# Kernel tuning notes

Measured on AMD Instinct MI355X. Metric: run time of the kernel, lower is better.

## Reference

```python
import jax, jax.numpy as jnp
import numpy as np
import math

B, T, D, NH, HD = 2, 1024, 768, 12, 64
V, L, E, CAP_F, H = 50257, 2, 8, 1.25, 2048
AUX_W, Z_W, THETA, EPS = 0.01, 0.001, 10000.0, 1e-5
N = B * T
CAP = int(math.ceil(N / E * CAP_F))  # 320


def setup_inputs():
    key = jax.random.key(0)
    ks = jax.random.split(key, 8)
    s = 0.02
    return dict(
        idx=jax.random.randint(ks[0], (B, T), 0, V),
        wte=jax.random.normal(ks[1], (V, D), jnp.float32) * s,
        wqkv=jax.random.normal(ks[2], (L, D, 3 * D), jnp.float32) * s,
        q_norm_w=jnp.ones((L, D), jnp.float32),
        k_norm_w=jnp.ones((L, D), jnp.float32),
        o_proj=jax.random.normal(ks[3], (L, D, D), jnp.float32) * s,
        ffn_norm_w=jnp.ones((L, D), jnp.float32),
        gate_w=jax.random.normal(ks[4], (L, D, E), jnp.float32) * s,
        w13=jax.random.normal(ks[5], (L, E, D, 2 * H), jnp.float32) * s,
        w2=jax.random.normal(ks[6], (L, E, H, D), jnp.float32) * s,
        ln_f_w=jnp.ones((D,), jnp.float32),
    )


def rmsnorm(x, w):
    return x * jax.lax.rsqrt(jnp.mean(x * x, axis=-1, keepdims=True) + EPS) * w


def rope(x, cos, sin):
    # x: (B, nh, T, HD) viewed as complex pairs on last dim
    xr = x.reshape(*x.shape[:-1], HD // 2, 2)
    x0, x1 = xr[..., 0], xr[..., 1]
    out = jnp.stack([x0 * cos - x1 * sin, x0 * sin + x1 * cos], axis=-1)
    return out.reshape(x.shape)


def moe(x, gate_w, w13, w2):
    # x: (B, T, D) -> Switch MoE (k=1) with capacity CAP and token drops
    x_flat = x.reshape(N, D).astype(jnp.float32)
    logits = x_flat @ gate_w  # (N, E) fp32
    probs = jax.nn.softmax(logits, axis=-1)
    top = jnp.argmax(logits, axis=-1)  # (N,)
    prob_mass = probs.mean(axis=0)
    fraction = jax.nn.one_hot(top, E, dtype=jnp.float32).mean(axis=0)
    balance_loss = jnp.sum(prob_mass * fraction) * AUX_W * E
    z = jax.nn.logsumexp(logits, axis=-1)
    z_loss = jnp.mean(z * z) * Z_W
    aux = balance_loss + z_loss

    sort_idx = jnp.argsort(top)  # stable
    sorted_assign = top[sort_idx]
    counts = jnp.bincount(sorted_assign, length=E)
    offsets = jnp.concatenate([jnp.zeros((1,), counts.dtype), jnp.cumsum(counts)])[:E]
    rank = jnp.arange(N) - offsets[sorted_assign]  # position within expert segment
    keep = rank < CAP
    x_perm = x_flat[sort_idx]
    slot = jnp.where(keep, rank, CAP)  # dropped -> overflow slot
    buf = jnp.zeros((E, CAP + 1, D), jnp.float32).at[sorted_assign, slot].set(x_perm)
    xb = buf[:, :CAP]  # (E, CAP, D)
    gu = jnp.einsum('ecd,edh->ech', xb, w13)  # (E, CAP, 2H)
    g, u = jnp.split(gu, 2, axis=-1)
    y = jnp.einsum('ech,ehd->ecd', jax.nn.silu(g) * u, w2)  # (E, CAP, D)
    out_perm = y[sorted_assign, jnp.minimum(rank, CAP - 1)] * keep[:, None]
    out_flat = jnp.zeros((N, D), jnp.float32).at[sort_idx].set(out_perm)
    return out_flat.reshape(B, T, D), aux, top.reshape(B, T), keep[jnp.argsort(sort_idx)].reshape(B, T)


def forward(idx, wte, wqkv, q_norm_w, k_norm_w, o_proj, ffn_norm_w, gate_w, w13, w2, ln_f_w):
    x = wte[idx]  # (B, T, D)
    freqs = 1.0 / (THETA ** (jnp.arange(0, HD, 2, dtype=jnp.float32) / HD))
    ang = jnp.outer(jnp.arange(T, dtype=jnp.float32), freqs)  # (T, HD//2)
    cos, sin = jnp.cos(ang)[None, None], jnp.sin(ang)[None, None]
    mask = jnp.where(jnp.tril(jnp.ones((T, T), bool)), 0.0, -jnp.inf)
    aux_total = jnp.float32(0.0)
    for l in range(L):
        qkv = x @ wqkv[l]
        q, k, v = jnp.split(qkv, 3, axis=-1)
        q = rmsnorm(q, q_norm_w[l])
        k = rmsnorm(k, k_norm_w[l])
        q = q.reshape(B, T, NH, HD).transpose(0, 2, 1, 3)
        k = k.reshape(B, T, NH, HD).transpose(0, 2, 1, 3)
        v = v.reshape(B, T, NH, HD).transpose(0, 2, 1, 3)
        q, k = rope(q, cos, sin), rope(k, cos, sin)
        scores = jnp.einsum('bhqd,bhkd->bhqk', q, k) / math.sqrt(HD) + mask
        attn = jax.nn.softmax(scores, axis=-1)
        y = jnp.einsum('bhqk,bhkd->bhqd', attn, v).transpose(0, 2, 1, 3).reshape(B, T, D)
        h = x + y @ o_proj[l]
        ffn_in = rmsnorm(h, ffn_norm_w[l])
        moe_out, aux, _, _ = moe(ffn_in, gate_w[l], w13[l], w2[l])
        aux_total = aux_total + aux
        x = h + moe_out
    x = rmsnorm(x, ln_f_w)
    logits = x @ wte.T  # tied lm_head
    return logits, aux_total


def reference(idx, wte, wqkv, q_norm_w, k_norm_w, o_proj, ffn_norm_w, gate_w, w13, w2, ln_f_w):
    return forward(idx, wte, wqkv, q_norm_w, k_norm_w, o_proj, ffn_norm_w, gate_w, w13, w2, ln_f_w)
```

## Files before the change

kernel.cpp:

```cpp
#include <hip/hip_runtime.h>

typedef __attribute__((ext_vector_type(8))) _Float16 half8;
typedef __attribute__((ext_vector_type(4))) float f32x4;

constexpr int Bc = 2, Tc = 1024, Dc = 768, NHc = 12, HDc = 64;
constexpr int Vc = 50257, Lc = 2, Ec = 8, Hc = 2048;
constexpr int Ntok = Bc * Tc;
constexpr int CAPc = 320, CAPPc = 384;
constexpr long long LOGITS_N = (long long)Bc * Tc * Vc;

typedef const __attribute__((address_space(1))) unsigned int* gas_t;
typedef __attribute__((address_space(3))) unsigned int* las_t;
__device__ __forceinline__ void gload16(const void* g, void* l) {
  __builtin_amdgcn_global_load_lds((gas_t)g, (las_t)l, 16, 0, 0);
}

__device__ __forceinline__ void splitf16(float a, unsigned short& h, unsigned short& l) {
  _Float16 hh = (_Float16)a;
  _Float16 ll = (_Float16)(a - (float)hh);
  h = __builtin_bit_cast(unsigned short, hh);
  l = __builtin_bit_cast(unsigned short, ll);
}
__device__ __forceinline__ unsigned short f16o(float a) {
  _Float16 hh = (_Float16)a;
  return __builtin_bit_cast(unsigned short, hh);
}


__global__ void zero_small(float* psum, float* z2) {
  int t = threadIdx.x;
  if (t < Lc * Ec) psum[t] = 0.f;
  if (t < Lc) z2[t] = 0.f;
}

__global__ void embed_k(const int* __restrict__ idx, const float* __restrict__ wte,
                        float* __restrict__ x, unsigned short* __restrict__ x16) {
  int n = blockIdx.x;
  long long v = idx[n];
  const float4* src = (const float4*)(wte + v * 768);
  float4* dst = (float4*)(x + (long long)n * 768);
  int t = threadIdx.x;
  if (t < 192) {
    float4 val = src[t];
    dst[t] = val;
    ushort4 h, l;
    splitf16(val.x, h.x, l.x); splitf16(val.y, h.y, l.y);
    splitf16(val.z, h.z, l.z); splitf16(val.w, h.w, l.w);
    unsigned short* d = x16 + (long long)n * 1536 + t * 4;
    *(ushort4*)d = h;
    *(ushort4*)(d + 768) = l;
  }
}

__global__ void f2h4(const float* __restrict__ in, unsigned short* __restrict__ out,
                     long long n4) {
  long long i = (long long)blockIdx.x * 256 + threadIdx.x;
  if (i >= n4) return;
  float4 v = ((const float4*)in)[i];
  ushort4 o;
  o.x = f16o(v.x); o.y = f16o(v.y); o.z = f16o(v.z); o.w = f16o(v.w);
  ((ushort4*)out)[i] = o;
}

template <int SP>
__global__ void __launch_bounds__(256) split2_wT(const float* __restrict__ src,
    unsigned short* __restrict__ dst, int K, int N, long long sS, long long sD) {
  __shared__ float t[32][33];
  int z = blockIdx.z;
  src += (long long)z * sS;
  dst += (long long)z * sD;
  int n0 = blockIdx.x * 32, k0 = blockIdx.y * 32;
  int tid = threadIdx.x;
  int r = tid >> 3, c4 = (tid & 7) * 4;
  float4 v = *(const float4*)(src + (long long)(k0 + r) * N + n0 + c4);
  t[r][c4 + 0] = v.x; t[r][c4 + 1] = v.y; t[r][c4 + 2] = v.z; t[r][c4 + 3] = v.w;
  __syncthreads();
  int n = tid >> 3, kq = (tid & 7) * 4;
  ushort4 h, l;
  splitf16(t[kq + 0][n], h.x, l.x);
  splitf16(t[kq + 1][n], h.y, l.y);
  splitf16(t[kq + 2][n], h.z, l.z);
  splitf16(t[kq + 3][n], h.w, l.w);
  const int lda = SP ? 2 * K : K;
  unsigned short* d = dst + (long long)(n0 + n) * lda + k0 + kq;
  *(ushort4*)d = h;
  if (SP) *(ushort4*)(d + K) = l;
}

__global__ void __launch_bounds__(256) rmsnorm_k(const float* in, int istride,
                                                 float* outp, int ostride,
                                                 const float* w) {
  long long n = blockIdx.x;
  const float* xr = in + n * istride;
  float* yr = outp + n * ostride;
  int tid = threadIdx.x;
  float s = 0.f;
  for (int i = tid; i < 768; i += 256) { float v = xr[i]; s += v * v; }
  #pragma unroll
  for (int o = 32; o; o >>= 1) s += __shfl_down(s, o);
  __shared__ float red[4];
  __shared__ float bs;
  if ((tid & 63) == 0) red[tid >> 6] = s;
  __syncthreads();
  if (tid == 0) bs = rsqrtf((red[0] + red[1] + red[2] + red[3]) / 768.0f + 1e-5f);
  __syncthreads();
  float sc = bs;
  for (int i = tid; i < 768; i += 256) yr[i] = xr[i] * sc * w[i];
}

__global__ void __launch_bounds__(256) rmsnorm_h(const float* in,
                                                 unsigned short* outp, const float* w) {
  long long n = blockIdx.x;
  const float* xr = in + n * 768;
  unsigned short* yr = outp + n * 768;
  int tid = threadIdx.x;
  float s = 0.f;
  for (int i = tid; i < 768; i += 256) { float v = xr[i]; s += v * v; }
  #pragma unroll
  for (int o = 32; o; o >>= 1) s += __shfl_down(s, o);
  __shared__ float red[4];
  __shared__ float bs;
  if ((tid & 63) == 0) red[tid >> 6] = s;
  __syncthreads();
  if (tid == 0) bs = rsqrtf((red[0] + red[1] + red[2] + red[3]) / 768.0f + 1e-5f);
  __syncthreads();
  float sc = bs;
  for (int i = tid; i < 768; i += 256) yr[i] = f16o(xr[i] * sc * w[i]);
}

__global__ void __launch_bounds__(256) qk_rope(const float* __restrict__ qkv,
    const float* __restrict__ qnw, const float* __restrict__ knw,
    unsigned short* __restrict__ qr, unsigned short* __restrict__ kr,
    unsigned short* __restrict__ vr) {
  int n = blockIdx.x;
  int t = n & 1023, b = n >> 10;
  const float* row = qkv + (long long)n * 2304;
  int tid = threadIdx.x;
  float sq = 0.f, sk = 0.f;
  for (int i = tid; i < 768; i += 256) {
    float q = row[i]; sq += q * q;
    float k = row[768 + i]; sk += k * k;
  }
  #pragma unroll
  for (int o = 32; o; o >>= 1) { sq += __shfl_down(sq, o); sk += __shfl_down(sk, o); }
  __shared__ float redq[4], redk[4];
  __shared__ float bq, bk;
  if ((tid & 63) == 0) { redq[tid >> 6] = sq; redk[tid >> 6] = sk; }
  __syncthreads();
  if (tid == 0) {
    bq = rsqrtf((redq[0] + redq[1] + redq[2] + redq[3]) / 768.0f + 1e-5f);
    bk = rsqrtf((redk[0] + redk[1] + redk[2] + redk[3]) / 768.0f + 1e-5f);
  }
  __syncthreads();
  float nq = bq, nk = bk;
  for (int i = tid; i < 384; i += 256) {
    int hh = i >> 5, j = i & 31;
    int c = hh * 64 + 2 * j;
    float ang = (float)t * powf(10000.0f, -((float)j * (1.0f / 32.0f)));
    float cs = cosf(ang), sn = sinf(ang);
    int z = b * 12 + hh;
    long long qb = ((long long)z * 1024 + t) * 128 + 2 * j;
    unsigned short h0, l0, h1, l1;
    float q0 = row[c] * nq * qnw[c], q1 = row[c + 1] * nq * qnw[c + 1];
    splitf16(q0 * cs - q1 * sn, h0, l0);
    splitf16(q0 * sn + q1 * cs, h1, l1);
    *(unsigned int*)&qr[qb] = (unsigned)h0 | ((unsigned)h1 << 16);
    *(unsigned int*)&qr[qb + 64] = (unsigned)l0 | ((unsigned)l1 << 16);
    float k0 = row[768 + c] * nk * knw[c], k1 = row[768 + c + 1] * nk * knw[c + 1];
    splitf16(k0 * cs - k1 * sn, h0, l0);
    splitf16(k0 * sn + k1 * cs, h1, l1);
    *(unsigned int*)&kr[qb] = (unsigned)h0 | ((unsigned)h1 << 16);
    *(unsigned int*)&kr[qb + 64] = (unsigned)l0 | ((unsigned)l1 << 16);
    splitf16(row[1536 + c], h0, l0);
    splitf16(row[1536 + c + 1], h1, l1);
    long long vb = ((long long)z * 64 + 2 * j) * 2048 + t;
    vr[vb] = h0; vr[vb + 1024] = l0;
    vr[vb + 2048] = h1; vr[vb + 3072] = l1;
  }
}

__global__ void __launch_bounds__(256) flash_attn(
    const unsigned short* __restrict__ qr, const unsigned short* __restrict__ kr,
    const unsigned short* __restrict__ vr, unsigned short* __restrict__ yout) {
  __shared__ __align__(16) unsigned short Ph[4][16][72];
  __shared__ __align__(16) unsigned short Pl[4][16][72];
  int bid = blockIdx.x;
  int z = bid >> 4;
  int qt = 15 - (bid & 15);
  int b = z / 12, h = z % 12;
  int q0 = qt * 64;
  int wave = threadIdx.x >> 6, lane = threadIdx.x & 63;
  int lr = lane & 15, lg = lane >> 4;
  int qw = q0 + wave * 16;
  half8 af[2][2];
  const unsigned short* qbase = qr + ((long long)z * 1024 + qw + lr) * 128;
  #pragma unroll
  for (int ks = 0; ks < 2; ++ks)
    #pragma unroll
    for (int p = 0; p < 2; ++p)
      af[ks][p] = *(const half8*)(qbase + p * 64 + ks * 32 + lg * 8);
  f32x4 accy[4];
  #pragma unroll
  for (int df = 0; df < 4; ++df) accy[df] = (f32x4){0.f, 0.f, 0.f, 0.f};
  float mrun[4] = {-3.4e38f, -3.4e38f, -3.4e38f, -3.4e38f};
  float srun[4] = {0.f, 0.f, 0.f, 0.f};
  for (int kt = 0; kt <= qt; ++kt) {
    int kv0 = kt * 64;
    f32x4 s[4];
    #pragma unroll
    for (int nf = 0; nf < 4; ++nf) s[nf] = (f32x4){0.f, 0.f, 0.f, 0.f};
    const unsigned short* kbase = kr + ((long long)z * 1024 + kv0 + lr) * 128;
    #pragma unroll
    for (int nf = 0; nf < 4; ++nf) {
      const unsigned short* kb = kbase + nf * 16 * 128;
      #pragma unroll
      for (int ks = 0; ks < 2; ++ks) {
        half8 bh = *(const half8*)(kb + ks * 32 + lg * 8);
        half8 bl = *(const half8*)(kb + 64 + ks * 32 + lg * 8);
        s[nf] = __builtin_amdgcn_mfma_f32_16x16x32_f16(af[ks][0], bh, s[nf], 0, 0, 0);
        s[nf] = __builtin_amdgcn_mfma_f32_16x16x32_f16(af[ks][1], bh, s[nf], 0, 0, 0);
        s[nf] = __builtin_amdgcn_mfma_f32_16x16x32_f16(af[ks][0], bl, s[nf], 0, 0, 0);
      }
    }
    bool diag = (kt == qt);
    #pragma unroll
    for (int nf = 0; nf < 4; ++nf)
      #pragma unroll
      for (int j = 0; j < 4; ++j) {
        float v = s[nf][j] * 0.125f;
        if (diag && (nf * 16 + lr > wave * 16 + lg * 4 + j)) v = -1e30f;
        s[nf][j] = v;
      }
    #pragma unroll
    for (int j = 0; j < 4; ++j) {
      float tm = fmaxf(fmaxf(s[0][j], s[1][j]), fmaxf(s[2][j], s[3][j]));
      #pragma unroll
      for (int o = 1; o < 16; o <<= 1) tm = fmaxf(tm, __shfl_xor(tm, o));
      float mnew = fmaxf(mrun[j], tm);
      float sc = expf(mrun[j] - mnew);
      float ts = 0.f;
      #pragma unroll
      for (int nf = 0; nf < 4; ++nf) {
        float p = expf(s[nf][j] - mnew);
        ts += p;
        unsigned short ph, pl;
        splitf16(p, ph, pl);
        Ph[wave][lg * 4 + j][nf * 16 + lr] = ph;
        Pl[wave][lg * 4 + j][nf * 16 + lr] = pl;
      }
      #pragma unroll
      for (int o = 1; o < 16; o <<= 1) ts += __shfl_xor(ts, o);
      srun[j] = srun[j] * sc + ts;
      mrun[j] = mnew;
      #pragma unroll
      for (int df = 0; df < 4; ++df) accy[df][j] *= sc;
    }
    #pragma unroll
    for (int ks2 = 0; ks2 < 2; ++ks2) {
      half8 aph = *(const half8*)&Ph[wave][lr][ks2 * 32 + lg * 8];
      half8 apl = *(const half8*)&Pl[wave][lr][ks2 * 32 + lg * 8];
      #pragma unroll
      for (int df = 0; df < 4; ++df) {
        const unsigned short* vb =
            vr + ((long long)z * 64 + df * 16 + lr) * 2048 + kv0 + ks2 * 32 + lg * 8;
        half8 bvh = *(const half8*)vb;
        half8 bvl = *(const half8*)(vb + 1024);
        accy[df] = __builtin_amdgcn_mfma_f32_16x16x32_f16(aph, bvh, accy[df], 0, 0, 0);
        accy[df] = __builtin_amdgcn_mfma_f32_16x16x32_f16(apl, bvh, accy[df], 0, 0, 0);
        accy[df] = __builtin_amdgcn_mfma_f32_16x16x32_f16(aph, bvl, accy[df], 0, 0, 0);
      }
    }
  }
  float inv[4];
  #pragma unroll
  for (int j = 0; j < 4; ++j) inv[j] = 1.0f / srun[j];
  #pragma unroll
  for (int df = 0; df < 4; ++df)
    #pragma unroll
    for (int j = 0; j < 4; ++j) {
      long long tok = (long long)b * 1024 + qw + lg * 4 + j;
      int col = h * 64 + df * 16 + lr;
      unsigned short hh, ll;
      splitf16(accy[df][j] * inv[j], hh, ll);
      yout[tok * 1536 + col] = hh;
      yout[tok * 1536 + 768 + col] = ll;
    }
}

__global__ void __launch_bounds__(256) gate_k(const float* __restrict__ xin,
    const float* __restrict__ gw, int* __restrict__ top,
    float* __restrict__ psum, float* __restrict__ z2) {
  __shared__ float gws[768 * 8];
  __shared__ float pacc[8];
  __shared__ float zacc;
  int tid = threadIdx.x;
  for (int i = tid; i < 768 * 8 / 4; i += 256) ((float4*)gws)[i] = ((const float4*)gw)[i];
  if (tid < 8) pacc[tid] = 0.f;
  if (tid == 0) zacc = 0.f;
  __syncthreads();
  int n = blockIdx.x * 256 + tid;
  const float4* xr4 = (const float4*)(xin + (long long)n * 768);
  float l[8] = {0, 0, 0, 0, 0, 0, 0, 0};
  for (int d4 = 0; d4 < 192; ++d4) {
    float4 xv = xr4[d4];
    const float* g = &gws[d4 * 32];
    #pragma unroll
    for (int e = 0; e < 8; ++e)
      l[e] += xv.x * g[e] + xv.y * g[8 + e] + xv.z * g[16 + e] + xv.w * g[24 + e];
  }
  float mx = l[0]; int bi = 0;
  #pragma unroll
  for (int e = 1; e < 8; ++e) if (l[e] > mx) { mx = l[e]; bi = e; }
  float p[8]; float se = 0.f;
  #pragma unroll
  for (int e = 0; e < 8; ++e) { p[e] = expf(l[e] - mx); se += p[e]; }
  float z = mx + logf(se);
  top[n] = bi;
  #pragma unroll
  for (int e = 0; e < 8; ++e) atomicAdd(&pacc[e], p[e] / se);
  atomicAdd(&zacc, z * z);
  __syncthreads();
  if (tid < 8) atomicAdd(&psum[tid], pacc[tid]);
  if (tid == 0) atomicAdd(z2, zacc);
}

__global__ void route_scan(const int* __restrict__ top, int* __restrict__ rank,
                           int* __restrict__ cnt) {
  int lane = threadIdx.x;
  int c[8] = {0, 0, 0, 0, 0, 0, 0, 0};
  unsigned long long below = (1ull << lane) - 1ull;
  for (int s = 0; s < Ntok / 64; ++s) {
    int n = s * 64 + lane;
    int e = top[n];
    int r = 0;
    #pragma unroll
    for (int q = 0; q < 8; ++q) {
      unsigned long long m = __ballot(e == q);
      if (e == q) r = c[q] + __popcll(m & below);
      c[q] += __popcll(m);
    }
    rank[n] = r;
  }
  #pragma unroll
  for (int q = 0; q < 8; ++q) if (lane == q) cnt[q] = c[q];
}

template <int SP>
__global__ void scatter_xb(const float* __restrict__ xin, const int* __restrict__ top,
                           const int* __restrict__ rank, unsigned short* __restrict__ xb) {
  int n = blockIdx.x;
  int r = rank[n];
  if (r >= CAPc) return;
  int e = top[n];
  int t = threadIdx.x;
  if (t >= 192) return;
  float4 v = ((const float4*)(xin + (long long)n * 768))[t];
  ushort4 h, l;
  splitf16(v.x, h.x, l.x); splitf16(v.y, h.y, l.y);
  splitf16(v.z, h.z, l.z); splitf16(v.w, h.w, l.w);
  const int lda = SP ? 1536 : 768;
  unsigned short* dst = xb + ((long long)e * CAPPc + r) * lda + t * 4;
  *(ushort4*)dst = h;
  if (SP) *(ushort4*)(dst + 768) = l;
}

template <int SP>
__global__ void __launch_bounds__(256) silu_k(const float* __restrict__ gu,
                                              unsigned short* __restrict__ act) {
  long long i = (long long)blockIdx.x * 256 + threadIdx.x;
  long long row = i >> 11;
  int h = (int)(i & 2047);
  float g = gu[row * 4096 + h];
  float u = gu[row * 4096 + 2048 + h];
  float a = g / (1.f + expf(-g)) * u;
  if (SP) {
    unsigned short hh, ll;
    splitf16(a, hh, ll);
    act[row * 4096 + h] = hh;
    act[row * 4096 + 2048 + h] = ll;
  } else {
    act[row * 2048 + h] = f16o(a);
  }
}

__global__ void gather_add(const float* __restrict__ h, const float* __restrict__ yexp,
                           const int* __restrict__ top, const int* __restrict__ rank,
                           float* __restrict__ xo, unsigned short* __restrict__ x16) {
  int n = blockIdx.x;
  int r = rank[n], e = top[n];
  bool kept = r < CAPc;
  int rc = kept ? r : (CAPc - 1);
  const float4* hs = (const float4*)(h + (long long)n * 768);
  const float4* ys = (const float4*)(yexp + ((long long)e * CAPPc + rc) * 768);
  float4* dst = (float4*)(xo + (long long)n * 768);
  int t = threadIdx.x;
  if (t < 192) {
    float4 v = hs[t];
    if (kept) { float4 y = ys[t]; v.x += y.x; v.y += y.y; v.z += y.z; v.w += y.w; }
    dst[t] = v;
    ushort4 hh, ll;
    splitf16(v.x, hh.x, ll.x); splitf16(v.y, hh.y, ll.y);
    splitf16(v.z, hh.z, ll.z); splitf16(v.w, hh.w, ll.w);
    unsigned short* d = x16 + (long long)n * 1536 + t * 4;
    *(ushort4*)d = hh;
    *(ushort4*)(d + 768) = ll;
  }
}

__global__ void aux_fin(const float* __restrict__ psum, const int* __restrict__ cnt,
                        const float* __restrict__ z2, float* __restrict__ outp) {
  if (threadIdx.x == 0) {
    float aux = 0.f;
    for (int l = 0; l < Lc; ++l) {
      float bl = 0.f;
      for (int e = 0; e < 8; ++e)
        bl += (psum[l * 8 + e] * (1.0f / 2048.0f)) * ((float)cnt[l * 8 + e] * (1.0f / 2048.0f));
      aux += bl * (0.01f * 8.0f) + (z2[l] * (1.0f / 2048.0f)) * 0.001f;
    }
    outp[0] = aux;
  }
}

template <int BN, int SPLIT, int ADD, int NTAIL>
__global__ void __launch_bounds__(256) gemm_h(
    const unsigned short* __restrict__ A, const unsigned short* __restrict__ Bt,
    float* __restrict__ C, const float* __restrict__ Add,
    int M, int N, int K, int ldc, int gx, int gy,
    long long sA, long long sB, int zdiv, long long sC1, long long sC2) {
  constexpr int FN = (BN == 128) ? 4 : 2;
  __shared__ __align__(16) unsigned short Ash[128 * 32];
  __shared__ __align__(16) unsigned short Asl[128 * 32];
  __shared__ __align__(16) unsigned short Bsh[BN * 32];
  __shared__ __align__(16) unsigned short Bsl[BN * 32];
  int tot = gridDim.x;
  int lin = blockIdx.x;
  if ((tot & 7) == 0) lin = (lin & 7) * (tot >> 3) + (lin >> 3);
  int pz = lin / (gx * gy);
  int r2 = lin - pz * (gx * gy);
  const int m0 = (r2 % gx) * 128, n0 = (r2 / gx) * BN;
  A += (long long)pz * sA;
  Bt += (long long)pz * sB;
  const long long co = (long long)(pz / zdiv) * sC1 + (long long)(pz % zdiv) * sC2;
  const int lda = SPLIT ? 2 * K : K;
  const int NS = SPLIT ? K / 32 : K / 64;
  const int tid = threadIdx.x;
  const int lane = tid & 63, wave = tid >> 6;
  const int wm = (BN == 128) ? (wave >> 1) : (wave & 1);
  const int wn = (BN == 128) ? (wave & 1) : (wave >> 1);
  const int srow = tid >> 2, scol = (tid & 3) * 8;
  const unsigned short* Ar = A + (long long)(m0 + srow) * lda + scol;
  int br0 = n0 + srow;
  if (NTAIL) br0 = min(br0, N - 1);
  const unsigned short* Br = Bt + (long long)br0 * lda + scol;
  int br1 = n0 + srow + 64;
  if (NTAIL) br1 = min(br1, N - 1);
  const unsigned short* Br2 = Bt + (long long)br1 * lda + scol;
  f32x4 acc[4][FN];
  #pragma unroll
  for (int m = 0; m < 4; ++m)
    #pragma unroll
    for (int n = 0; n < FN; ++n) acc[m][n] = (f32x4){0.f, 0.f, 0.f, 0.f};
  for (int s = 0; s < NS; ++s) {
    const int kh = SPLIT ? s * 32 : s * 64;
    const int kl = SPLIT ? K + s * 32 : s * 64 + 32;
    gload16(Ar + kh, &Ash[wave * 512]);
    gload16(Ar + (long long)64 * lda + kh, &Ash[2048 + wave * 512]);
    gload16(Ar + kl, &Asl[wave * 512]);
    gload16(Ar + (long long)64 * lda + kl, &Asl[2048 + wave * 512]);
    gload16(Br + kh, &Bsh[wave * 512]);
    gload16(Br + kl, &Bsl[wave * 512]);
    if (BN == 128) {
      gload16(Br2 + kh, &Bsh[2048 + wave * 512]);
      gload16(Br2 + kl, &Bsl[2048 + wave * 512]);
    }
    __syncthreads();
    half8 bfh[FN], bfl[FN];
    #pragma unroll
    for (int n = 0; n < FN; ++n) {
      int bo = (wn * (FN * 16) + n * 16 + (lane & 15)) * 32 + (lane >> 4) * 8;
      bfh[n] = *(const half8*)&Bsh[bo];
      bfl[n] = *(const half8*)&Bsl[bo];
    }
    #pragma unroll
    for (int m = 0; m < 4; ++m) {
      int ao = (wm * 64 + m * 16 + (lane & 15)) * 32 + (lane >> 4) * 8;
      half8 afh = *(const half8*)&Ash[ao];
      half8 afl = *(const half8*)&Asl[ao];
      #pragma unroll
      for (int n = 0; n < FN; ++n) {
        acc[m][n] = __builtin_amdgcn_mfma_f32_16x16x32_f16(afh, bfh[n], acc[m][n], 0, 0, 0);
        if (SPLIT) {
          acc[m][n] = __builtin_amdgcn_mfma_f32_16x16x32_f16(afl, bfh[n], acc[m][n], 0, 0, 0);
          acc[m][n] = __builtin_amdgcn_mfma_f32_16x16x32_f16(afh, bfl[n], acc[m][n], 0, 0, 0);
        } else {
          acc[m][n] = __builtin_amdgcn_mfma_f32_16x16x32_f16(afl, bfl[n], acc[m][n], 0, 0, 0);
        }
      }
    }
    __syncthreads();
  }
  #pragma unroll
  for (int m = 0; m < 4; ++m)
    #pragma unroll
    for (int n = 0; n < FN; ++n) {
      int col = n0 + wn * (FN * 16) + n * 16 + (lane & 15);
      if (!NTAIL || col < N) {
        #pragma unroll
        for (int j = 0; j < 4; ++j) {
          long long row = m0 + wm * 64 + m * 16 + (lane >> 4) * 4 + j;
          long long o = co + row * ldc + col;
          float v = acc[m][n][j];
          if (ADD) v += Add[o];
          C[o] = v;
        }
      }
    }
}


extern "C" void kernel_launch(void* const* d_in, const int* in_sizes, int n_in,
                              void* d_out, int out_size, void* d_ws, size_t ws_size,
                              hipStream_t stream) {
  (void)in_sizes; (void)n_in; (void)out_size; (void)ws_size;
  const int*   idx   = (const int*)d_in[0];
  const float* wte   = (const float*)d_in[1];
  const float* wqkv  = (const float*)d_in[2];
  const float* qnw   = (const float*)d_in[3];
  const float* knw   = (const float*)d_in[4];
  const float* oproj = (const float*)d_in[5];
  const float* ffnw  = (const float*)d_in[6];
  const float* gatew = (const float*)d_in[7];
  const float* w13   = (const float*)d_in[8];
  const float* w2p   = (const float*)d_in[9];
  const float* lnf   = (const float*)d_in[10];
  float* out = (float*)d_out;

  char* base = (char*)d_ws;
  size_t off = 0;
  auto alloc = [&](size_t bytes) -> char* {
    off = (off + 255) & ~(size_t)255;
    char* p = base + off; off += bytes; return p;
  };
  float* x     = (float*)alloc((size_t)Ntok * 768 * 4);
  float* qkv   = (float*)alloc((size_t)Ntok * 2304 * 4);
  float* hbuf  = (float*)alloc((size_t)Ntok * 768 * 4);
  float* ffn   = (float*)alloc((size_t)Ntok * 768 * 4);
  unsigned short* x16   = (unsigned short*)alloc((size_t)Ntok * 1536 * 2);
  unsigned short* yfl16 = (unsigned short*)alloc((size_t)Ntok * 1536 * 2);
  unsigned short* qr16  = (unsigned short*)alloc((size_t)24 * 1024 * 128 * 2);
  unsigned short* kr16  = (unsigned short*)alloc((size_t)24 * 1024 * 128 * 2);
  unsigned short* vr16  = (unsigned short*)alloc((size_t)24 * 64 * 2048 * 2);
  unsigned short* xb16  = (unsigned short*)alloc((size_t)Ec * CAPPc * 1536 * 2);
  unsigned short* wo16  = (unsigned short*)alloc((size_t)768 * 1536 * 2);
  unsigned short* xf16  = (unsigned short*)alloc((size_t)Ntok * 768 * 2);
  char* spb = alloc((size_t)24 * 1024 * 1024 * 4);
  float* gu   = (float*)spb;
  float* yexp = (float*)spb;
  unsigned short* act16 = (unsigned short*)(spb + 50331648);
  unsigned short* wq16  = (unsigned short*)(spb + 75497472);
  unsigned short* w13_16 = (unsigned short*)alloc((size_t)Ec * 4096 * 1536 * 2);
  unsigned short* wt16   = w13_16;
  unsigned short* w2_16  = (unsigned short*)alloc((size_t)Ec * 768 * 4096 * 2);
  int* top    = (int*)alloc(Ntok * 4);
  int* rankb  = (int*)alloc(Ntok * 4);
  int* cnt    = (int*)alloc(Lc * Ec * 4);
  float* psum = (float*)alloc(Lc * Ec * 4);
  float* z2   = (float*)alloc(Lc * 4);

  zero_small<<<1, 64, 0, stream>>>(psum, z2);
  embed_k<<<Ntok, 192, 0, stream>>>(idx, wte, x, x16);

  for (int l = 0; l < Lc; ++l) {
    split2_wT<1><<<dim3(72, 24, 1), 256, 0, stream>>>(wqkv + (size_t)l * 768 * 2304, wq16,
                                                      768, 2304, 0, 0);
    split2_wT<1><<<dim3(24, 24, 1), 256, 0, stream>>>(oproj + (size_t)l * 768 * 768, wo16,
                                                      768, 768, 0, 0);
    if (l == 0) {
      split2_wT<1><<<dim3(128, 24, 8), 256, 0, stream>>>(w13, w13_16,
          768, 4096, (long long)768 * 4096, (long long)4096 * 1536);
      split2_wT<1><<<dim3(24, 64, 8), 256, 0, stream>>>(w2p, w2_16,
          2048, 768, (long long)2048 * 768, (long long)768 * 4096);
    } else {
      split2_wT<0><<<dim3(128, 24, 8), 256, 0, stream>>>(w13 + (size_t)Ec * 768 * 4096, w13_16,
          768, 4096, (long long)768 * 4096, (long long)4096 * 768);
      split2_wT<0><<<dim3(24, 64, 8), 256, 0, stream>>>(w2p + (size_t)Ec * 2048 * 768, w2_16,
          2048, 768, (long long)2048 * 768, (long long)768 * 2048);
    }
    gemm_h<128, 1, 0, 0><<<288, 256, 0, stream>>>(
        x16, wq16, qkv, nullptr, 2048, 2304, 768, 2304, 16, 18, 0, 0, 1, 0, 0);
    qk_rope<<<Ntok, 256, 0, stream>>>(qkv, qnw + l * 768, knw + l * 768, qr16, kr16, vr16);
    flash_attn<<<384, 256, 0, stream>>>(qr16, kr16, vr16, yfl16);
    gemm_h<64, 1, 1, 0><<<192, 256, 0, stream>>>(
        yfl16, wo16, hbuf, x, 2048, 768, 768, 768, 16, 12, 0, 0, 1, 0, 0);
    rmsnorm_k<<<Ntok, 256, 0, stream>>>(hbuf, 768, ffn, 768, ffnw + l * 768);
    gate_k<<<Ntok / 256, 256, 0, stream>>>(ffn, gatew + (size_t)l * 768 * 8, top,
                                           psum + l * 8, z2 + l);
    route_scan<<<1, 64, 0, stream>>>(top, rankb, cnt + l * 8);
    if (l == 0) {
      scatter_xb<1><<<Ntok, 192, 0, stream>>>(ffn, top, rankb, xb16);
      gemm_h<128, 1, 0, 0><<<768, 256, 0, stream>>>(
          xb16, w13_16, gu, nullptr, 384, 4096, 768, 4096, 3, 32,
          (long long)384 * 1536, (long long)4096 * 1536, 1, (long long)384 * 4096, 0);
      silu_k<1><<<(Ec * CAPPc * Hc) / 256, 256, 0, stream>>>(gu, act16);
      gemm_h<64, 1, 0, 0><<<288, 256, 0, stream>>>(
          act16, w2_16, yexp, nullptr, 384, 768, 2048, 768, 3, 12,
          (long long)384 * 4096, (long long)768 * 4096, 1, (long long)384 * 768, 0);
    } else {
      scatter_xb<0><<<Ntok, 192, 0, stream>>>(ffn, top, rankb, xb16);
      gemm_h<128, 0, 0, 0><<<768, 256, 0, stream>>>(
          xb16, w13_16, gu, nullptr, 384, 4096, 768, 4096, 3, 32,
          (long long)384 * 768, (long long)4096 * 768, 1, (long long)384 * 4096, 0);
      silu_k<0><<<(Ec * CAPPc * Hc) / 256, 256, 0, stream>>>(gu, act16);
      gemm_h<64, 0, 0, 0><<<288, 256, 0, stream>>>(
          act16, w2_16, yexp, nullptr, 384, 768, 2048, 768, 3, 12,
          (long long)384 * 2048, (long long)768 * 2048, 1, (long long)384 * 768, 0);
    }
    gather_add<<<Ntok, 192, 0, stream>>>(hbuf, yexp, top, rankb, x, x16);
  }

  rmsnorm_h<<<Ntok, 256, 0, stream>>>(x, xf16, lnf);
  f2h4<<<(int)(((long long)Vc * 768 / 4 + 255) / 256), 256, 0, stream>>>(
      wte, wt16, (long long)Vc * 768 / 4);
  gemm_h<128, 0, 0, 1><<<6288, 256, 0, stream>>>(
      xf16, wt16, out, nullptr, 2048, Vc, 768, Vc, 16, 393, 0, 0, 1, 0, 0);
  aux_fin<<<1, 64, 0, stream>>>(psum, cnt, z2, out + LOGITS_N);
}
```

Before: 1.346 ms.

## Double-buffer LDS tiles in split-f16 GEMM and raise MFMA wave priority

Converts the GEMM main loop from single-buffered LDS staging to a two-buffer ping-pong, issuing async global-to-LDS loads for the next K-step before the MFMAs on the current one. This removes one barrier per iteration and is meant to overlap global memory latency with matrix compute. It also raises wave priority around the MFMA block with s_setprio. LDS use per block doubles, which can lower occupancy. With one barrier per step, correctness relies on the async LDS loads being complete when the barrier is reached.

```diff
diff --git a/kernel.cpp b/kernel.cpp
--- a/kernel.cpp
+++ b/kernel.cpp
@@ -428,10 +428,10 @@
     int M, int N, int K, int ldc, int gx, int gy,
     long long sA, long long sB, int zdiv, long long sC1, long long sC2) {
   constexpr int FN = (BN == 128) ? 4 : 2;
-  __shared__ __align__(16) unsigned short Ash[128 * 32];
-  __shared__ __align__(16) unsigned short Asl[128 * 32];
-  __shared__ __align__(16) unsigned short Bsh[BN * 32];
-  __shared__ __align__(16) unsigned short Bsl[BN * 32];
+  constexpr int APL = 128 * 32;
+  constexpr int BPL = BN * 32;
+  constexpr int BUF = 2 * APL + 2 * BPL;
+  __shared__ __align__(16) unsigned short lds[2][BUF];
   int tot = gridDim.x;
   int lin = blockIdx.x;
   if ((tot & 7) == 0) lin = (lin & 7) * (tot >> 3) + (lin >> 3);
@@ -455,37 +455,48 @@
   int br1 = n0 + srow + 64;
   if (NTAIL) br1 = min(br1, N - 1);
   const unsigned short* Br2 = Bt + (long long)br1 * lda + scol;
-  f32x4 acc[4][FN];
-  #pragma unroll
-  for (int m = 0; m < 4; ++m)
-    #pragma unroll
-    for (int n = 0; n < FN; ++n) acc[m][n] = (f32x4){0.f, 0.f, 0.f, 0.f};
-  for (int s = 0; s < NS; ++s) {
+
+  auto STAGE = [&](int buf, int s) {
     const int kh = SPLIT ? s * 32 : s * 64;
     const int kl = SPLIT ? K + s * 32 : s * 64 + 32;
-    gload16(Ar + kh, &Ash[wave * 512]);
-    gload16(Ar + (long long)64 * lda + kh, &Ash[2048 + wave * 512]);
-    gload16(Ar + kl, &Asl[wave * 512]);
-    gload16(Ar + (long long)64 * lda + kl, &Asl[2048 + wave * 512]);
-    gload16(Br + kh, &Bsh[wave * 512]);
-    gload16(Br + kl, &Bsl[wave * 512]);
+    unsigned short* L = lds[buf];
+    gload16(Ar + kh, &L[wave * 512]);
+    gload16(Ar + (long long)64 * lda + kh, &L[2048 + wave * 512]);
+    gload16(Ar + kl, &L[APL + wave * 512]);
+    gload16(Ar + (long long)64 * lda + kl, &L[APL + 2048 + wave * 512]);
+    gload16(Br + kh, &L[2 * APL + wave * 512]);
+    gload16(Br + kl, &L[2 * APL + BPL + wave * 512]);
     if (BN == 128) {
-      gload16(Br2 + kh, &Bsh[2048 + wave * 512]);
-      gload16(Br2 + kl, &Bsl[2048 + wave * 512]);
-    }
-    __syncthreads();
+      gload16(Br2 + kh, &L[2 * APL + 2048 + wave * 512]);
+      gload16(Br2 + kl, &L[2 * APL + BPL + 2048 + wave * 512]);
+    }
+  };
+
+  f32x4 acc[4][FN];
+  #pragma unroll
+  for (int m = 0; m < 4; ++m)
+    #pragma unroll
+    for (int n = 0; n < FN; ++n) acc[m][n] = (f32x4){0.f, 0.f, 0.f, 0.f};
+
+  STAGE(0, 0);
+  __syncthreads();
+  int cur = 0;
+  for (int s = 0; s < NS; ++s) {
+    if (s + 1 < NS) STAGE(cur ^ 1, s + 1);
+    const unsigned short* L = lds[cur];
     half8 bfh[FN], bfl[FN];
     #pragma unroll
     for (int n = 0; n < FN; ++n) {
       int bo = (wn * (FN * 16) + n * 16 + (lane & 15)) * 32 + (lane >> 4) * 8;
-      bfh[n] = *(const half8*)&Bsh[bo];
-      bfl[n] = *(const half8*)&Bsl[bo];
-    }
+      bfh[n] = *(const half8*)&L[2 * APL + bo];
+      bfl[n] = *(const half8*)&L[2 * APL + BPL + bo];
+    }
+    __builtin_amdgcn_s_setprio(1);
     #pragma unroll
     for (int m = 0; m < 4; ++m) {
       int ao = (wm * 64 + m * 16 + (lane & 15)) * 32 + (lane >> 4) * 8;
-      half8 afh = *(const half8*)&Ash[ao];
-      half8 afl = *(const half8*)&Asl[ao];
+      half8 afh = *(const half8*)&L[ao];
+      half8 afl = *(const half8*)&L[APL + ao];
       #pragma unroll
       for (int n = 0; n < FN; ++n) {
         acc[m][n] = __builtin_amdgcn_mfma_f32_16x16x32_f16(afh, bfh[n], acc[m][n], 0, 0, 0);
@@ -497,7 +508,9 @@
         }
       }
     }
+    __builtin_amdgcn_s_setprio(0);
     __syncthreads();
+    cur ^= 1;
   }
   #pragma unroll
   for (int m = 0; m < 4; ++m)
```

Result: no change. 1.336 ms (-0.7%).
